# Performance work log

Hardware: AMD Instinct MI355X
Metric: run time of the kernel (lower is better)

## Reference

```python
import jax, jax.numpy as jnp
import numpy as np

N_NODES = 50000
D = 64            # encoder.out_node_dim
N_EDGES = 800000
HID = 64          # mlp_edge_model_dim


def setup_inputs() -> dict:
    key = jax.random.key(0)
    k1, k2, k3, k4 = jax.random.split(key, 4)
    node_emb = jax.random.normal(k1, (N_NODES, D), dtype=jnp.float32)
    edge_index = jax.random.randint(k2, (2, N_EDGES), 0, N_NODES, dtype=jnp.int64)
    # Xavier-uniform style init for the 2-layer edge MLP
    lim1 = np.sqrt(6.0 / (2 * D + HID)).astype(np.float32)
    lim2 = np.sqrt(6.0 / (HID + 1)).astype(np.float32)
    W1 = jax.random.uniform(k3, (2 * D, HID), minval=-lim1, maxval=lim1, dtype=jnp.float32)
    b1 = jnp.zeros((HID,), dtype=jnp.float32)
    W2 = jax.random.uniform(k4, (HID, 1), minval=-lim2, maxval=lim2, dtype=jnp.float32)
    b2 = jnp.zeros((1,), dtype=jnp.float32)
    return {"node_emb": node_emb, "edge_index": edge_index,
            "W1": W1, "b1": b1, "W2": W2, "b2": b2}


def reference(node_emb, edge_index, W1, b1, W2, b2):
    src, dst = edge_index[0], edge_index[1]
    emb_src = node_emb[src]              # [E, D] gather
    emb_dst = node_emb[dst]              # [E, D] gather
    edge_emb = jnp.concatenate([emb_src, emb_dst], axis=1)  # [E, 2D]
    h = jax.nn.relu(edge_emb @ W1 + b1)  # [E, HID]
    edge_logits = h @ W2 + b2            # [E, 1]
    return edge_logits
```

## Files before the change

kernel.cpp:

```cpp
#include <hip/hip_runtime.h>


typedef __attribute__((ext_vector_type(8))) short short8;
typedef __attribute__((ext_vector_type(4))) float f32x4;
typedef __attribute__((ext_vector_type(8))) _Float16 half8;

__device__ __forceinline__ unsigned short f2bf_rne(float f) {
    union { float f; unsigned u; } v;
    v.f = f;
    return (unsigned short)((v.u + 0x7FFFu + ((v.u >> 16) & 1u)) >> 16);
}

#define W1T_K 72
#define CT_STRIDE 136

__global__ __launch_bounds__(256)
void node_uv(const float* __restrict__ X,
             const float* __restrict__ W1,
             const float* __restrict__ b1,
             _Float16* __restrict__ UV,
             int nnodes, int ntiles) {
    __shared__ __align__(16) unsigned short w1t[128 * W1T_K];
    __shared__ __align__(16) _Float16 cbuf[4][16 * CT_STRIDE];

    const int tid = threadIdx.x;
#pragma unroll
    for (int i = 0; i < 32; ++i) {
        int idx = tid + i * 256;
        int r = idx >> 6;
        int col = idx & 63;
        int k = r & 63;
        int jp = col + (r & 64);
        w1t[jp * W1T_K + k] = f2bf_rne(W1[idx]);
    }
    __syncthreads();

    const int lane = tid & 63;
    const int wid = tid >> 6;
    const int c = lane & 15;
    const int quad = lane >> 4;

    const int t = blockIdx.x * 4 + wid;
    if (t >= ntiles) return;

    short8 bfrag[8][2];
#pragma unroll
    for (int nt = 0; nt < 8; ++nt)
#pragma unroll
        for (int kc = 0; kc < 2; ++kc)
            bfrag[nt][kc] =
                *(const short8*)&w1t[(nt * 16 + c) * W1T_K + kc * 32 + quad * 8];

    float b1v[8];
#pragma unroll
    for (int nt = 0; nt < 8; ++nt)
        b1v[nt] = (nt < 4) ? b1[nt * 16 + c] : 0.f;

    int n = t * 16 + c;
    n = (n < nnodes) ? n : (nnodes - 1);
    const float* xr = X + (size_t)n * 64 + quad * 8;
    f32x4 x0a = *(const f32x4*)(xr);
    f32x4 x0b = *(const f32x4*)(xr + 4);
    f32x4 x1a = *(const f32x4*)(xr + 32);
    f32x4 x1b = *(const f32x4*)(xr + 36);
    short8 a0, a1;
#pragma unroll
    for (int i = 0; i < 4; ++i) {
        a0[i] = (short)f2bf_rne(x0a[i]);
        a0[4 + i] = (short)f2bf_rne(x0b[i]);
        a1[i] = (short)f2bf_rne(x1a[i]);
        a1[4 + i] = (short)f2bf_rne(x1b[i]);
    }

    f32x4 acc[8];
#pragma unroll
    for (int nt = 0; nt < 8; ++nt) acc[nt] = (f32x4){0.f, 0.f, 0.f, 0.f};
#pragma unroll
    for (int nt = 0; nt < 8; ++nt) {
        acc[nt] = __builtin_amdgcn_mfma_f32_16x16x32_bf16(a0, bfrag[nt][0], acc[nt], 0, 0, 0);
        acc[nt] = __builtin_amdgcn_mfma_f32_16x16x32_bf16(a1, bfrag[nt][1], acc[nt], 0, 0, 0);
    }

    _Float16* cb = cbuf[wid];
#pragma unroll
    for (int nt = 0; nt < 8; ++nt)
#pragma unroll
        for (int r = 0; r < 4; ++r)
            cb[(quad * 4 + r) * CT_STRIDE + nt * 16 + c] =
                (_Float16)(acc[nt][r] + b1v[nt]);

    __builtin_amdgcn_s_waitcnt(0);

    const _Float16* rp = &cb[(lane >> 2) * CT_STRIDE + (lane & 3) * 32];
    const f32x4* s4 = (const f32x4*)rp;
    f32x4* dst = (f32x4*)(UV + (size_t)t * 2048 + lane * 32);
    dst[0] = s4[0];
    dst[1] = s4[1];
    dst[2] = s4[2];
    dst[3] = s4[3];
}

__global__ __launch_bounds__(256)
void edge_out(const int* __restrict__ eidx,
              const _Float16* __restrict__ UV,
              const float* __restrict__ W2,
              const float* __restrict__ b2,
              float* __restrict__ out, int E) {
    int tid = blockIdx.x * 256 + threadIdx.x;
    int e = tid >> 3;
    int j = tid & 7;
    if (e >= E) return;

    int src = eidx[e];
    int dst = eidx[E + e];

    half8 u = *(const half8*)(UV + (size_t)src * 128 + j * 8);
    half8 v = *(const half8*)(UV + (size_t)dst * 128 + 64 + j * 8);
    f32x4 w2a = *(const f32x4*)(W2 + j * 8);
    f32x4 w2b = *(const f32x4*)(W2 + j * 8 + 4);

    float acc = 0.f;
#pragma unroll
    for (int i = 0; i < 4; ++i) {
        float h0 = fmaxf((float)u[i] + (float)v[i], 0.f);
        float h1 = fmaxf((float)u[4 + i] + (float)v[4 + i], 0.f);
        acc = fmaf(h0, w2a[i], acc);
        acc = fmaf(h1, w2b[i], acc);
    }
    acc += __shfl_xor(acc, 1, 8);
    acc += __shfl_xor(acc, 2, 8);
    acc += __shfl_xor(acc, 4, 8);
    if (j == 0) out[e] = acc + b2[0];
}

extern "C" void kernel_launch(void* const* d_in, const int* in_sizes, int n_in,
                              void* d_out, int out_size, void* d_ws, size_t ws_size,
                              hipStream_t stream) {
    const float* X = (const float*)d_in[0];
    const int* eidx = (const int*)d_in[1];
    const float* W1 = (const float*)d_in[2];
    const float* b1 = (const float*)d_in[3];
    const float* W2 = (const float*)d_in[4];
    const float* b2 = (const float*)d_in[5];
    float* out = (float*)d_out;

    const int nnodes = in_sizes[0] / 64;
    const int E = in_sizes[1] / 2;

    _Float16* UV = (_Float16*)d_ws;

    const int ntiles = (nnodes + 15) / 16;
    node_uv<<<(ntiles + 3) / 4, 256, 0, stream>>>(X, W1, b1, UV, nnodes, ntiles);

    const int nthreads = E * 8;
    edge_out<<<(nthreads + 255) / 256, 256, 0, stream>>>(eidx, UV, W2, b2, out, E);
}
```

Measured before the change: 104.0 us.

## Fuse node projection and edge scoring into one persistent cooperative kernel

Merges the node_uv and edge_out kernels into a single persistent kernel launched cooperatively and sized to occupancy. Node tiles and edges are processed with grid-stride loops, separated by a grid-wide sync. This removes the second launch and the gap between kernels, and spreads the W1 LDS staging across fewer blocks. In exchange it adds the cost of a grid barrier, limits the edge phase to the resident grid size, and reloads B fragments from LDS on every tile.

Measured after the change: 289.1 us. 2.78x slower.

```diff
diff --git a/kernel.cpp b/kernel.cpp
--- a/kernel.cpp
+++ b/kernel.cpp
@@ -1,4 +1,7 @@
 #include <hip/hip_runtime.h>
+#include <hip/hip_cooperative_groups.h>
+
+namespace cg = cooperative_groups;
 
 
 typedef __attribute__((ext_vector_type(8))) short short8;
@@ -14,12 +17,16 @@
 #define W1T_K 72
 #define CT_STRIDE 136
 
-__global__ __launch_bounds__(256)
-void node_uv(const float* __restrict__ X,
-             const float* __restrict__ W1,
-             const float* __restrict__ b1,
-             _Float16* __restrict__ UV,
-             int nnodes, int ntiles) {
+__global__ __launch_bounds__(256, 4)
+void fused(const float* __restrict__ X,
+           const int* __restrict__ eidx,
+           const float* __restrict__ W1,
+           const float* __restrict__ b1,
+           const float* __restrict__ W2,
+           const float* __restrict__ b2,
+           _Float16* __restrict__ UV,
+           float* __restrict__ out,
+           int nnodes, int ntiles, int E) {
     __shared__ __align__(16) unsigned short w1t[128 * W1T_K];
     __shared__ __align__(16) _Float16 cbuf[4][16 * CT_STRIDE];
 
@@ -40,97 +47,87 @@
     const int c = lane & 15;
     const int quad = lane >> 4;
 
-    const int t = blockIdx.x * 4 + wid;
-    if (t >= ntiles) return;
-
-    short8 bfrag[8][2];
-#pragma unroll
-    for (int nt = 0; nt < 8; ++nt)
-#pragma unroll
-        for (int kc = 0; kc < 2; ++kc)
-            bfrag[nt][kc] =
-                *(const short8*)&w1t[(nt * 16 + c) * W1T_K + kc * 32 + quad * 8];
-
     float b1v[8];
 #pragma unroll
     for (int nt = 0; nt < 8; ++nt)
         b1v[nt] = (nt < 4) ? b1[nt * 16 + c] : 0.f;
 
-    int n = t * 16 + c;
-    n = (n < nnodes) ? n : (nnodes - 1);
-    const float* xr = X + (size_t)n * 64 + quad * 8;
-    f32x4 x0a = *(const f32x4*)(xr);
-    f32x4 x0b = *(const f32x4*)(xr + 4);
-    f32x4 x1a = *(const f32x4*)(xr + 32);
-    f32x4 x1b = *(const f32x4*)(xr + 36);
-    short8 a0, a1;
+    for (int t = blockIdx.x * 4 + wid; t < ntiles; t += gridDim.x * 4) {
+        int n = t * 16 + c;
+        n = (n < nnodes) ? n : (nnodes - 1);
+        const float* xr = X + (size_t)n * 64 + quad * 8;
+        f32x4 x0a = *(const f32x4*)(xr);
+        f32x4 x0b = *(const f32x4*)(xr + 4);
+        f32x4 x1a = *(const f32x4*)(xr + 32);
+        f32x4 x1b = *(const f32x4*)(xr + 36);
+        short8 a0, a1;
 #pragma unroll
-    for (int i = 0; i < 4; ++i) {
-        a0[i] = (short)f2bf_rne(x0a[i]);
-        a0[4 + i] = (short)f2bf_rne(x0b[i]);
-        a1[i] = (short)f2bf_rne(x1a[i]);
-        a1[4 + i] = (short)f2bf_rne(x1b[i]);
+        for (int i = 0; i < 4; ++i) {
+            a0[i] = (short)f2bf_rne(x0a[i]);
+            a0[4 + i] = (short)f2bf_rne(x0b[i]);
+            a1[i] = (short)f2bf_rne(x1a[i]);
+            a1[4 + i] = (short)f2bf_rne(x1b[i]);
+        }
+
+        f32x4 acc[8];
+#pragma unroll
+        for (int nt = 0; nt < 8; ++nt) {
+            short8 bf0 = *(const short8*)&w1t[(nt * 16 + c) * W1T_K + 0 * 32 + quad * 8];
+            short8 bf1 = *(const short8*)&w1t[(nt * 16 + c) * W1T_K + 1 * 32 + quad * 8];
+            acc[nt] = (f32x4){0.f, 0.f, 0.f, 0.f};
+            acc[nt] = __builtin_amdgcn_mfma_f32_16x16x32_bf16(a0, bf0, acc[nt], 0, 0, 0);
+            acc[nt] = __builtin_amdgcn_mfma_f32_16x16x32_bf16(a1, bf1, acc[nt], 0, 0, 0);
+        }
+
+        _Float16* cb = cbuf[wid];
+#pragma unroll
+        for (int nt = 0; nt < 8; ++nt)
+#pragma unroll
+            for (int r = 0; r < 4; ++r)
+                cb[(quad * 4 + r) * CT_STRIDE + nt * 16 + c] =
+                    (_Float16)(acc[nt][r] + b1v[nt]);
+
+        __builtin_amdgcn_s_waitcnt(0);
+
+        const _Float16* rp = &cb[(lane >> 2) * CT_STRIDE + (lane & 3) * 32];
+        const f32x4* s4 = (const f32x4*)rp;
+        f32x4* dstp = (f32x4*)(UV + (size_t)t * 2048 + lane * 32);
+        dstp[0] = s4[0];
+        dstp[1] = s4[1];
+        dstp[2] = s4[2];
+        dstp[3] = s4[3];
     }
 
-    f32x4 acc[8];
+    __threadfence();
+    cg::this_grid().sync();
+
+    const int v0 = blockIdx.x * 256 + tid;
+    const int j = v0 & 7;
+    const f32x4 w2a = *(const f32x4*)(W2 + j * 8);
+    const f32x4 w2b = *(const f32x4*)(W2 + j * 8 + 4);
+    const float b2v = b2[0];
+    const int estep = (gridDim.x * 256) >> 3;
+
+    for (int e = v0 >> 3; e < E; e += estep) {
+        int sidx = eidx[e];
+        int didx = eidx[E + e];
+
+        half8 u = *(const half8*)(UV + (size_t)sidx * 128 + j * 8);
+        half8 v = *(const half8*)(UV + (size_t)didx * 128 + 64 + j * 8);
+
+        float acc = 0.f;
 #pragma unroll
-    for (int nt = 0; nt < 8; ++nt) acc[nt] = (f32x4){0.f, 0.f, 0.f, 0.f};
-#pragma unroll
-    for (int nt = 0; nt < 8; ++nt) {
-        acc[nt] = __builtin_amdgcn_mfma_f32_16x16x32_bf16(a0, bfrag[nt][0], acc[nt], 0, 0, 0);
-        acc[nt] = __builtin_amdgcn_mfma_f32_16x16x32_bf16(a1, bfrag[nt][1], acc[nt], 0, 0, 0);
+        for (int i = 0; i < 4; ++i) {
+            float h0 = fmaxf((float)u[i] + (float)v[i], 0.f);
+            float h1 = fmaxf((float)u[4 + i] + (float)v[4 + i], 0.f);
+            acc = fmaf(h0, w2a[i], acc);
+            acc = fmaf(h1, w2b[i], acc);
+        }
+        acc += __shfl_xor(acc, 1, 8);
+        acc += __shfl_xor(acc, 2, 8);
+        acc += __shfl_xor(acc, 4, 8);
+        if (j == 0) out[e] = acc + b2v;
     }
-
-    _Float16* cb = cbuf[wid];
-#pragma unroll
-    for (int nt = 0; nt < 8; ++nt)
-#pragma unroll
-        for (int r = 0; r < 4; ++r)
-            cb[(quad * 4 + r) * CT_STRIDE + nt * 16 + c] =
-                (_Float16)(acc[nt][r] + b1v[nt]);
-
-    __builtin_amdgcn_s_waitcnt(0);
-
-    const _Float16* rp = &cb[(lane >> 2) * CT_STRIDE + (lane & 3) * 32];
-    const f32x4* s4 = (const f32x4*)rp;
-    f32x4* dst = (f32x4*)(UV + (size_t)t * 2048 + lane * 32);
-    dst[0] = s4[0];
-    dst[1] = s4[1];
-    dst[2] = s4[2];
-    dst[3] = s4[3];
-}
-
-__global__ __launch_bounds__(256)
-void edge_out(const int* __restrict__ eidx,
-              const _Float16* __restrict__ UV,
-              const float* __restrict__ W2,
-              const float* __restrict__ b2,
-              float* __restrict__ out, int E) {
-    int tid = blockIdx.x * 256 + threadIdx.x;
-    int e = tid >> 3;
-    int j = tid & 7;
-    if (e >= E) return;
-
-    int src = eidx[e];
-    int dst = eidx[E + e];
-
-    half8 u = *(const half8*)(UV + (size_t)src * 128 + j * 8);
-    half8 v = *(const half8*)(UV + (size_t)dst * 128 + 64 + j * 8);
-    f32x4 w2a = *(const f32x4*)(W2 + j * 8);
-    f32x4 w2b = *(const f32x4*)(W2 + j * 8 + 4);
-
-    float acc = 0.f;
-#pragma unroll
-    for (int i = 0; i < 4; ++i) {
-        float h0 = fmaxf((float)u[i] + (float)v[i], 0.f);
-        float h1 = fmaxf((float)u[4 + i] + (float)v[4 + i], 0.f);
-        acc = fmaf(h0, w2a[i], acc);
-        acc = fmaf(h1, w2b[i], acc);
-    }
-    acc += __shfl_xor(acc, 1, 8);
-    acc += __shfl_xor(acc, 2, 8);
-    acc += __shfl_xor(acc, 4, 8);
-    if (j == 0) out[e] = acc + b2[0];
 }
 
 extern "C" void kernel_launch(void* const* d_in, const int* in_sizes, int n_in,
@@ -149,9 +146,23 @@
 
     _Float16* UV = (_Float16*)d_ws;
 
-    const int ntiles = (nnodes + 15) / 16;
-    node_uv<<<(ntiles + 3) / 4, 256, 0, stream>>>(X, W1, b1, UV, nnodes, ntiles);
+    int ntiles = (nnodes + 15) / 16;
 
-    const int nthreads = E * 8;
-    edge_out<<<(nthreads + 255) / 256, 256, 0, stream>>>(eidx, UV, W2, b2, out, E);
+    static int gridsz = 0;
+    if (gridsz == 0) {
+        int dev = 0;
+        (void)hipGetDevice(&dev);
+        hipDeviceProp_t prop;
+        (void)hipGetDeviceProperties(&prop, dev);
+        int nb = 0;
+        (void)hipOccupancyMaxActiveBlocksPerMultiprocessor(&nb, fused, 256, 0);
+        if (nb < 1) nb = 1;
+        gridsz = nb * prop.multiProcessorCount;
+    }
+
+    void* args[] = {(void*)&X, (void*)&eidx, (void*)&W1, (void*)&b1,
+                    (void*)&W2, (void*)&b2, (void*)&UV, (void*)&out,
+                    (void*)&nnodes, (void*)&ntiles, (void*)&E};
+    (void)hipLaunchCooperativeKernel((void*)fused, dim3(gridsz), dim3(256),
+                                     args, 0, stream);
 }
```
